# Kernel tuning notes

Hardware: AMD Instinct MI355X
Metric: run time of the kernel (lower is better)

## Reference

```python
import jax, jax.numpy as jnp
import numpy as np

N = 100000          # nodes of type 'note'
E = 800000          # edges per relation
D = 128             # in_feat == hidden_channels
NUM_LAYERS = 3
NUM_REL = 3         # onset, consecutive, during


def setup_inputs() -> dict:
    key = jax.random.key(0)
    ks = jax.random.split(key, 12)
    inp = {
        "x": jax.random.normal(ks[0], (N, D), dtype=jnp.float32),
        "edge_index_onset": jax.random.randint(ks[1], (2, E), 0, N, dtype=jnp.int64),
        "edge_index_consecutive": jax.random.randint(ks[2], (2, E), 0, N, dtype=jnp.int64),
        "edge_index_during": jax.random.randint(ks[3], (2, E), 0, N, dtype=jnp.int64),
        # hop masks: sorted node hops (seeds first), edge hops in [0, num_layers]
        "node_mask": jnp.sort(jax.random.randint(ks[4], (N,), 0, NUM_LAYERS + 1, dtype=jnp.int64)),
        "edge_mask_onset": jax.random.randint(ks[5], (E,), 0, NUM_LAYERS + 1, dtype=jnp.int64),
        "edge_mask_consecutive": jax.random.randint(ks[6], (E,), 0, NUM_LAYERS + 1, dtype=jnp.int64),
        "edge_mask_during": jax.random.randint(ks[7], (E,), 0, NUM_LAYERS + 1, dtype=jnp.int64),
        # SAGEConv weights per (layer, relation): lin_l (with bias) on aggregated
        # neighbor mean, lin_r (no bias) on root features.
        "W_l": jax.random.normal(ks[8], (NUM_LAYERS, NUM_REL, D, D), dtype=jnp.float32) / np.sqrt(D),
        "b_l": jnp.zeros((NUM_LAYERS, NUM_REL, D), dtype=jnp.float32),
        "W_r": jax.random.normal(ks[9], (NUM_LAYERS, NUM_REL, D, D), dtype=jnp.float32) / np.sqrt(D),
    }
    return inp


def _hetero_sage_forward(x, edge_indices, node_mask, edge_masks, W_l, b_l, W_r):
    h = x
    for i in range(NUM_LAYERS):
        layer = NUM_LAYERS - i  # trim_to_layer(layer=num_layers - i, ...)
        nvalid = node_mask <= layer                      # [N] kept nodes this layer
        out = jnp.zeros((N, D), dtype=h.dtype)
        for t in range(NUM_REL):
            src, dst = edge_indices[t][0], edge_indices[t][1]
            evalid = (edge_masks[t] <= layer).astype(h.dtype)  # [E] kept edges
            msg = h[src] * evalid[:, None]                     # gather + mask  [E, D]
            agg = jax.ops.segment_sum(msg, dst, num_segments=N)          # [N, D]
            cnt = jax.ops.segment_sum(evalid, dst, num_segments=N)       # [N]
            mean = agg / jnp.maximum(cnt, 1.0)[:, None]
            # SAGEConv: lin_l(mean) + lin_r(x_root); HeteroConv aggr='sum' over relations
            out = out + mean @ W_l[i, t].T + b_l[i, t] + h @ W_r[i, t].T
        h = jnp.where(nvalid[:, None], jax.nn.relu(out), 0.0)
    return h


def reference(x, edge_index_onset, edge_index_consecutive, edge_index_during,
              node_mask, edge_mask_onset, edge_mask_consecutive, edge_mask_during,
              W_l, b_l, W_r):
    edge_indices = (edge_index_onset, edge_index_consecutive, edge_index_during)
    edge_masks = (edge_mask_onset, edge_mask_consecutive, edge_mask_during)
    return _hetero_sage_forward(x, edge_indices, node_mask, edge_masks, W_l, b_l, W_r)
```

## Files before the change

kernel.cpp:

```cpp
#include <hip/hip_runtime.h>

#define N_NODES 100000
#define N_EDGES 800000
#define D 128
#define SCAN_N (4 * N_NODES)
#define SCAN_TOTAL (3 * SCAN_N)
#define SCAN_CHUNK 2048
#define SCAN_BLOCKS 586
#define SCAN_PAD (SCAN_BLOCKS * SCAN_CHUNK)

typedef _Float16 f16x8 __attribute__((ext_vector_type(8)));
typedef _Float16 f16x4 __attribute__((ext_vector_type(4)));
typedef float f32x4 __attribute__((ext_vector_type(4)));

#define MFMA_F16(a, b, c) __builtin_amdgcn_mfma_f32_16x16x32_f16((a), (b), (c), 0, 0, 0)

#define CONV_BLOCKS 12500
#define COUNT_BLOCKS 9375
#define PREPW_BLOCKS 768

__global__ __launch_bounds__(256) void prep_all(
    const float* __restrict__ x, _Float16* __restrict__ h,
    const int* __restrict__ ei0, const int* __restrict__ ei1, const int* __restrict__ ei2,
    const int* __restrict__ em0, const int* __restrict__ em1, const int* __restrict__ em2,
    int* __restrict__ cnt2, const float* __restrict__ W_l, const float* __restrict__ W_r,
    const float* __restrict__ b_l, _Float16* __restrict__ whi, float* __restrict__ bsum) {
    int b = blockIdx.x;
    int tid = threadIdx.x;
    if (b < CONV_BLOCKS) {
        int idx = b * 256 + tid;
        float4 v = reinterpret_cast<const float4*>(x)[idx];
        f16x4 o = {(_Float16)v.x, (_Float16)v.y, (_Float16)v.z, (_Float16)v.w};
        reinterpret_cast<f16x4*>(h)[idx] = o;
    } else if (b < CONV_BLOCKS + COUNT_BLOCKS) {
        int e = (b - CONV_BLOCKS) * 256 + tid;
        int r = e / N_EDGES;
        int el = e - r * N_EDGES;
        const int* ei = (r == 0) ? ei0 : (r == 1) ? ei1 : ei2;
        const int* em = (r == 0) ? em0 : (r == 1) ? em1 : em2;
        int dst = ei[N_EDGES + el];
        int m = em[el];
        atomicAdd(&cnt2[(size_t)r * SCAN_N + dst * 4 + m], 1);
    } else {
        int idx = (b - CONV_BLOCKS - COUNT_BLOCKS) * 256 + tid;
        if (idx < 3 * 4 * 16384) {
            int i = idx / (4 * 16384);
            int rem = idx % (4 * 16384);
            int slot = rem / 16384;
            int ok = rem % 16384;
            float v;
            if (slot < 3) {
                v = W_l[(size_t)(i * 3 + slot) * 16384 + ok];
            } else {
                const float* base = W_r + (size_t)i * 3 * 16384;
                v = base[ok] + base[16384 + ok] + base[2 * 16384 + ok];
            }
            whi[idx] = (_Float16)v;
        }
        if (idx < 3 * 128) {
            int i = idx / 128, o = idx % 128;
            const float* bb = b_l + (size_t)i * 3 * 128;
            bsum[idx] = bb[o] + bb[128 + o] + bb[256 + o];
        }
    }
}

__global__ __launch_bounds__(256) void scan_part(const int* __restrict__ cnt2,
                                                 int* __restrict__ bsums) {
    int tid = threadIdx.x;
    size_t base = (size_t)blockIdx.x * SCAN_CHUNK + tid * 8;
    int4 v0 = *reinterpret_cast<const int4*>(cnt2 + base);
    int4 v1 = *reinterpret_cast<const int4*>(cnt2 + base + 4);
    int s = v0.x + v0.y + v0.z + v0.w + v1.x + v1.y + v1.z + v1.w;
    __shared__ int red[256];
    red[tid] = s;
    __syncthreads();
    for (int off = 128; off > 0; off >>= 1) {
        if (tid < off) red[tid] += red[tid + off];
        __syncthreads();
    }
    if (tid == 0) bsums[blockIdx.x] = red[0];
}

__global__ __launch_bounds__(1024) void scan_tops(int* __restrict__ bsums) {
    __shared__ int s[1024];
    int tid = threadIdx.x;
    int v = (tid < SCAN_BLOCKS) ? bsums[tid] : 0;
    s[tid] = v;
    __syncthreads();
    for (int off = 1; off < 1024; off <<= 1) {
        int x = s[tid];
        int add = (tid >= off) ? s[tid - off] : 0;
        __syncthreads();
        s[tid] = x + add;
        __syncthreads();
    }
    if (tid < SCAN_BLOCKS) bsums[tid] = s[tid] - v;
}

__global__ __launch_bounds__(256) void scan_out(const int* __restrict__ cnt2,
                                                const int* __restrict__ bsums,
                                                int* __restrict__ bnd) {
    int tid = threadIdx.x;
    size_t base = (size_t)blockIdx.x * SCAN_CHUNK + tid * 8;
    int4 v0 = *reinterpret_cast<const int4*>(cnt2 + base);
    int4 v1 = *reinterpret_cast<const int4*>(cnt2 + base + 4);
    int l[8] = {v0.x, v0.y, v0.z, v0.w, v1.x, v1.y, v1.z, v1.w};
    int ts = l[0] + l[1] + l[2] + l[3] + l[4] + l[5] + l[6] + l[7];
    __shared__ int s[256];
    s[tid] = ts;
    __syncthreads();
    for (int off = 1; off < 256; off <<= 1) {
        int x = s[tid];
        int add = (tid >= off) ? s[tid - off] : 0;
        __syncthreads();
        s[tid] = x + add;
        __syncthreads();
    }
    int run = bsums[blockIdx.x] + s[tid] - ts;
    int o[8];
#pragma unroll
    for (int j = 0; j < 8; j++) {
        o[j] = run;
        run += l[j];
    }
    int4 o0 = {o[0], o[1], o[2], o[3]};
    int4 o1 = {o[4], o[5], o[6], o[7]};
    *reinterpret_cast<int4*>(bnd + base) = o0;
    *reinterpret_cast<int4*>(bnd + base + 4) = o1;
}

__global__ __launch_bounds__(256) void fill3(
    const int* __restrict__ ei0, const int* __restrict__ ei1, const int* __restrict__ ei2,
    const int* __restrict__ em0, const int* __restrict__ em1, const int* __restrict__ em2,
    const int* __restrict__ bnd, int* __restrict__ fill2, int* __restrict__ packed) {
    int e = blockIdx.x * 256 + threadIdx.x;
    int r = e / N_EDGES;
    int el = e - r * N_EDGES;
    const int* ei = (r == 0) ? ei0 : (r == 1) ? ei1 : ei2;
    const int* em = (r == 0) ? em0 : (r == 1) ? em1 : em2;
    int dst = ei[N_EDGES + el];
    int src = ei[el];
    int m = em[el];
    int gbk = r * SCAN_N + dst * 4 + m;
    int pos = bnd[gbk] + atomicAdd(&fill2[gbk], 1);
    packed[pos] = src * D;
}

__global__ __launch_bounds__(256, 8) void fused_layer(
    const _Float16* __restrict__ h_in, const int* __restrict__ bnd,
    const int* __restrict__ packed, const _Float16* __restrict__ Whi,
    const float* __restrict__ bias, const int* __restrict__ node_mask, int layer,
    _Float16* __restrict__ h_out, float* __restrict__ out_f32) {
    __shared__ __align__(16) _Float16 smean[3][32][136];
    int tid = threadIdx.x;
    int wid = tid >> 6;
    int lane = tid & 63;
    int row0 = blockIdx.x * 32;

    if (node_mask[row0] > layer) {
        if (out_f32) {
            f32x4 z = {0.f, 0.f, 0.f, 0.f};
            f32x4* o = reinterpret_cast<f32x4*>(out_f32 + (size_t)row0 * D);
#pragma unroll
            for (int k = 0; k < 4; k++) o[tid + k * 256] = z;
        } else {
            f16x8 z = (f16x8)(_Float16)0;
            f16x8* o = reinterpret_cast<f16x8*>(h_out + (size_t)row0 * D);
#pragma unroll
            for (int k = 0; k < 2; k++) o[tid + k * 256] = z;
        }
        return;
    }

    int g = lane >> 4;
    int l = lane & 15;

    const _Float16* hbase = h_in + l * 8;
#pragma unroll 1
    for (int it = 0; it < 6; it++) {
        int t = wid * 24 + it * 4 + g;
        int r = t >> 5;
        int n = t & 31;
        if (node_mask[row0 + n] > layer) continue;
        const int* B = bnd + (size_t)r * SCAN_N + (row0 + n) * 4;
        int beg = B[0];
        int end = B[layer + 1];
        int deg = end - beg;
        f16x8 acc = (f16x8)(_Float16)0;
#pragma unroll 1
        for (int e4 = beg & ~3; e4 < end; e4 += 4) {
            int4 s4 = *reinterpret_cast<const int4*>(packed + e4);
            if (e4 >= beg && e4 + 4 <= end) {
                f16x8 v0 = *reinterpret_cast<const f16x8*>(hbase + (size_t)(uint)s4.x);
                f16x8 v1 = *reinterpret_cast<const f16x8*>(hbase + (size_t)(uint)s4.y);
                f16x8 v2 = *reinterpret_cast<const f16x8*>(hbase + (size_t)(uint)s4.z);
                f16x8 v3 = *reinterpret_cast<const f16x8*>(hbase + (size_t)(uint)s4.w);
                acc += v0;
                acc += v1;
                acc += v2;
                acc += v3;
            } else {
                int ss[4] = {s4.x, s4.y, s4.z, s4.w};
#pragma unroll
                for (int j = 0; j < 4; j++) {
                    int e = e4 + j;
                    if (e >= beg && e < end)
                        acc += *reinterpret_cast<const f16x8*>(hbase + (size_t)(uint)ss[j]);
                }
            }
        }
        float inv = 1.f / fmaxf((float)deg, 1.f);
        f16x8 mv;
#pragma unroll
        for (int k = 0; k < 8; k++) mv[k] = (_Float16)((float)acc[k] * inv);
        *reinterpret_cast<f16x8*>(&smean[r][n][l * 8]) = mv;
    }
    __syncthreads();

    int colbase = wid * 32;
    int ln15 = lane & 15;
    int lg = lane >> 4;
    f32x4 acc[2][2] = {};

#pragma unroll
    for (int p = 0; p < 4; p++) {
        const _Float16* Whp = Whi + (size_t)p * 16384 + (size_t)colbase * D;
#pragma unroll
        for (int ks = 0; ks < 4; ks++) {
            int kof = ks * 32 + lg * 8;
            f16x8 a0f, a1f;
            if (p < 3) {
                a0f = *reinterpret_cast<const f16x8*>(&smean[p][ln15][kof]);
                a1f = *reinterpret_cast<const f16x8*>(&smean[p][16 + ln15][kof]);
            } else {
                a0f = *reinterpret_cast<const f16x8*>(h_in + (size_t)(row0 + ln15) * D + kof);
                a1f = *reinterpret_cast<const f16x8*>(h_in + (size_t)(row0 + 16 + ln15) * D + kof);
            }
            f16x8 bh0 = *reinterpret_cast<const f16x8*>(Whp + (size_t)ln15 * D + kof);
            f16x8 bh1 = *reinterpret_cast<const f16x8*>(Whp + (size_t)(16 + ln15) * D + kof);
            acc[0][0] = MFMA_F16(a0f, bh0, acc[0][0]);
            acc[0][1] = MFMA_F16(a0f, bh1, acc[0][1]);
            acc[1][0] = MFMA_F16(a1f, bh0, acc[1][0]);
            acc[1][1] = MFMA_F16(a1f, bh1, acc[1][1]);
        }
    }

#pragma unroll
    for (int r = 0; r < 2; r++)
#pragma unroll
        for (int j = 0; j < 4; j++) {
            int row = row0 + r * 16 + lg * 4 + j;
            bool valid = node_mask[row] <= layer;
#pragma unroll
            for (int cc = 0; cc < 2; cc++) {
                int col = colbase + cc * 16 + ln15;
                float v = acc[r][cc][j] + bias[col];
                v = valid ? fmaxf(v, 0.f) : 0.f;
                if (out_f32)
                    out_f32[(size_t)row * D + col] = v;
                else
                    h_out[(size_t)row * D + col] = (_Float16)v;
            }
        }
}

extern "C" void kernel_launch(void* const* d_in, const int* in_sizes, int n_in,
                              void* d_out, int out_size, void* d_ws, size_t ws_size,
                              hipStream_t stream) {
    const float* x = (const float*)d_in[0];
    const int* ei0 = (const int*)d_in[1];
    const int* ei1 = (const int*)d_in[2];
    const int* ei2 = (const int*)d_in[3];
    const int* node_mask = (const int*)d_in[4];
    const int* em0 = (const int*)d_in[5];
    const int* em1 = (const int*)d_in[6];
    const int* em2 = (const int*)d_in[7];
    const float* W_l = (const float*)d_in[8];
    const float* b_l = (const float*)d_in[9];
    const float* W_r = (const float*)d_in[10];

    _Float16* hA = (_Float16*)d_ws;
    _Float16* hB = hA + (size_t)N_NODES * D;
    _Float16* whi = hB + (size_t)N_NODES * D;
    float* bsum = (float*)(whi + 3 * 4 * 16384);
    int* cnt2 = (int*)(bsum + 3 * 128);
    int* fill2 = cnt2 + SCAN_PAD;
    int* bsums = fill2 + SCAN_TOTAL;
    int* bnd = bsums + 640;
    int* packed = bnd + SCAN_PAD;

    hipMemsetAsync(cnt2, 0, (size_t)(SCAN_PAD + SCAN_TOTAL) * sizeof(int), stream);

    prep_all<<<CONV_BLOCKS + COUNT_BLOCKS + PREPW_BLOCKS, 256, 0, stream>>>(
        x, hA, ei0, ei1, ei2, em0, em1, em2, cnt2, W_l, W_r, b_l, whi, bsum);
    scan_part<<<SCAN_BLOCKS, 256, 0, stream>>>(cnt2, bsums);
    scan_tops<<<1, 1024, 0, stream>>>(bsums);
    scan_out<<<SCAN_BLOCKS, 256, 0, stream>>>(cnt2, bsums, bnd);
    fill3<<<COUNT_BLOCKS, 256, 0, stream>>>(ei0, ei1, ei2, em0, em1, em2, bnd, fill2, packed);

    _Float16* hin = hA;
    _Float16* hout = hB;
    for (int i = 0; i < 3; i++) {
        int layer = 3 - i;
        float* of = (i == 2) ? (float*)d_out : nullptr;
        fused_layer<<<N_NODES / 32, 256, 0, stream>>>(
            hin, bnd, packed, whi + (size_t)i * 4 * 16384,
            bsum + (size_t)i * 128, node_mask, layer, hout, of);
        _Float16* tmp = hin; hin = hout; hout = tmp;
    }
}
```

Baseline: 631.9 us.

## Quantize node features to int8 per row for neighbor gather

```diff
diff --git a/kernel.cpp b/kernel.cpp
--- a/kernel.cpp
+++ b/kernel.cpp
@@ -11,6 +11,7 @@
 
 typedef _Float16 f16x8 __attribute__((ext_vector_type(8)));
 typedef _Float16 f16x4 __attribute__((ext_vector_type(4)));
+typedef _Float16 f16x2 __attribute__((ext_vector_type(2)));
 typedef float f32x4 __attribute__((ext_vector_type(4)));
 
 #define MFMA_F16(a, b, c) __builtin_amdgcn_mfma_f32_16x16x32_f16((a), (b), (c), 0, 0, 0)
@@ -65,6 +66,24 @@
     }
 }
 
+__global__ __launch_bounds__(256) void quant_rows(const _Float16* __restrict__ h,
+                                                  char* __restrict__ q,
+                                                  float* __restrict__ scales) {
+    int row = blockIdx.x * 4 + (threadIdx.x >> 6);
+    int lane = threadIdx.x & 63;
+    f16x2 v = *reinterpret_cast<const f16x2*>(h + (size_t)row * D + lane * 2);
+    float a0 = (float)v.x, a1 = (float)v.y;
+    float m = fmaxf(fabsf(a0), fabsf(a1));
+#pragma unroll
+    for (int off = 32; off; off >>= 1) m = fmaxf(m, __shfl_xor(m, off));
+    float k = (m > 0.f) ? 127.f / m : 0.f;
+    int q0 = (int)rintf(a0 * k);
+    int q1 = (int)rintf(a1 * k);
+    ushort pk = (ushort)((q0 & 0xFF) | ((q1 & 0xFF) << 8));
+    *reinterpret_cast<ushort*>(q + (size_t)row * D + lane * 2) = pk;
+    if (lane == 0) scales[row] = m * (1.f / 127.f);
+}
+
 __global__ __launch_bounds__(256) void scan_part(const int* __restrict__ cnt2,
                                                  int* __restrict__ bsums) {
     int tid = threadIdx.x;
@@ -147,8 +166,18 @@
     packed[pos] = src * D;
 }
 
-__global__ __launch_bounds__(256, 8) void fused_layer(
-    const _Float16* __restrict__ h_in, const int* __restrict__ bnd,
+__device__ __forceinline__ void acc8(float* a, uint2 b, float s) {
+#pragma unroll
+    for (int k = 0; k < 4; k++)
+        a[k] = fmaf(s, (float)((int)(b.x << (24 - 8 * k)) >> 24), a[k]);
+#pragma unroll
+    for (int k = 0; k < 4; k++)
+        a[4 + k] = fmaf(s, (float)((int)(b.y << (24 - 8 * k)) >> 24), a[4 + k]);
+}
+
+__global__ __launch_bounds__(256, 6) void fused_layer(
+    const _Float16* __restrict__ h_in, const char* __restrict__ q_in,
+    const float* __restrict__ scales, const int* __restrict__ bnd,
     const int* __restrict__ packed, const _Float16* __restrict__ Whi,
     const float* __restrict__ bias, const int* __restrict__ node_mask, int layer,
     _Float16* __restrict__ h_out, float* __restrict__ out_f32) {
@@ -176,7 +205,7 @@
     int g = lane >> 4;
     int l = lane & 15;
 
-    const _Float16* hbase = h_in + l * 8;
+    const char* qbase = q_in + l * 8;
 #pragma unroll 1
     for (int it = 0; it < 6; it++) {
         int t = wid * 24 + it * 4 + g;
@@ -187,33 +216,40 @@
         int beg = B[0];
         int end = B[layer + 1];
         int deg = end - beg;
-        f16x8 acc = (f16x8)(_Float16)0;
+        float a[8] = {};
 #pragma unroll 1
         for (int e4 = beg & ~3; e4 < end; e4 += 4) {
             int4 s4 = *reinterpret_cast<const int4*>(packed + e4);
             if (e4 >= beg && e4 + 4 <= end) {
-                f16x8 v0 = *reinterpret_cast<const f16x8*>(hbase + (size_t)(uint)s4.x);
-                f16x8 v1 = *reinterpret_cast<const f16x8*>(hbase + (size_t)(uint)s4.y);
-                f16x8 v2 = *reinterpret_cast<const f16x8*>(hbase + (size_t)(uint)s4.z);
-                f16x8 v3 = *reinterpret_cast<const f16x8*>(hbase + (size_t)(uint)s4.w);
-                acc += v0;
-                acc += v1;
-                acc += v2;
-                acc += v3;
+                uint2 b0 = *reinterpret_cast<const uint2*>(qbase + (size_t)(uint)s4.x);
+                uint2 b1 = *reinterpret_cast<const uint2*>(qbase + (size_t)(uint)s4.y);
+                uint2 b2 = *reinterpret_cast<const uint2*>(qbase + (size_t)(uint)s4.z);
+                uint2 b3 = *reinterpret_cast<const uint2*>(qbase + (size_t)(uint)s4.w);
+                float f0 = scales[(uint)s4.x >> 7];
+                float f1 = scales[(uint)s4.y >> 7];
+                float f2 = scales[(uint)s4.z >> 7];
+                float f3 = scales[(uint)s4.w >> 7];
+                acc8(a, b0, f0);
+                acc8(a, b1, f1);
+                acc8(a, b2, f2);
+                acc8(a, b3, f3);
             } else {
                 int ss[4] = {s4.x, s4.y, s4.z, s4.w};
 #pragma unroll
                 for (int j = 0; j < 4; j++) {
                     int e = e4 + j;
-                    if (e >= beg && e < end)
-                        acc += *reinterpret_cast<const f16x8*>(hbase + (size_t)(uint)ss[j]);
+                    if (e >= beg && e < end) {
+                        uint2 b = *reinterpret_cast<const uint2*>(qbase + (size_t)(uint)ss[j]);
+                        float f = scales[(uint)ss[j] >> 7];
+                        acc8(a, b, f);
+                    }
                 }
             }
         }
         float inv = 1.f / fmaxf((float)deg, 1.f);
         f16x8 mv;
 #pragma unroll
-        for (int k = 0; k < 8; k++) mv[k] = (_Float16)((float)acc[k] * inv);
+        for (int k = 0; k < 8; k++) mv[k] = (_Float16)(a[k] * inv);
         *reinterpret_cast<f16x8*>(&smean[r][n][l * 8]) = mv;
     }
     __syncthreads();
@@ -282,7 +318,11 @@
 
     _Float16* hA = (_Float16*)d_ws;
     _Float16* hB = hA + (size_t)N_NODES * D;
-    _Float16* whi = hB + (size_t)N_NODES * D;
+    char* qA = (char*)(hB + (size_t)N_NODES * D);
+    char* qB = qA + (size_t)N_NODES * D;
+    float* scA = (float*)(qB + (size_t)N_NODES * D);
+    float* scB = scA + N_NODES;
+    _Float16* whi = (_Float16*)(scB + N_NODES);
     float* bsum = (float*)(whi + 3 * 4 * 16384);
     int* cnt2 = (int*)(bsum + 3 * 128);
     int* fill2 = cnt2 + SCAN_PAD;
@@ -294,19 +334,20 @@
 
     prep_all<<<CONV_BLOCKS + COUNT_BLOCKS + PREPW_BLOCKS, 256, 0, stream>>>(
         x, hA, ei0, ei1, ei2, em0, em1, em2, cnt2, W_l, W_r, b_l, whi, bsum);
+    quant_rows<<<N_NODES / 4, 256, 0, stream>>>(hA, qA, scA);
     scan_part<<<SCAN_BLOCKS, 256, 0, stream>>>(cnt2, bsums);
     scan_tops<<<1, 1024, 0, stream>>>(bsums);
     scan_out<<<SCAN_BLOCKS, 256, 0, stream>>>(cnt2, bsums, bnd);
     fill3<<<COUNT_BLOCKS, 256, 0, stream>>>(ei0, ei1, ei2, em0, em1, em2, bnd, fill2, packed);
 
-    _Float16* hin = hA;
-    _Float16* hout = hB;
-    for (int i = 0; i < 3; i++) {
-        int layer = 3 - i;
-        float* of = (i == 2) ? (float*)d_out : nullptr;
-        fused_layer<<<N_NODES / 32, 256, 0, stream>>>(
-            hin, bnd, packed, whi + (size_t)i * 4 * 16384,
-            bsum + (size_t)i * 128, node_mask, layer, hout, of);
-        _Float16* tmp = hin; hin = hout; hout = tmp;
-    }
-}
+    fused_layer<<<N_NODES / 32, 256, 0, stream>>>(
+        hA, qA, scA, bnd, packed, whi, bsum, node_mask, 3, hB, nullptr);
+    quant_rows<<<N_NODES / 4, 256, 0, stream>>>(hB, qB, scB);
+    fused_layer<<<N_NODES / 32, 256, 0, stream>>>(
+        hB, qB, scB, bnd, packed, whi + (size_t)1 * 4 * 16384,
+        bsum + 128, node_mask, 2, hA, nullptr);
+    quant_rows<<<N_NODES / 4, 256, 0, stream>>>(hA, qA, scA);
+    fused_layer<<<N_NODES / 32, 256, 0, stream>>>(
+        hA, qA, scA, bnd, packed, whi + (size_t)2 * 4 * 16384,
+        bsum + 256, node_mask, 1, nullptr, (float*)d_out);
+}
```

Result: slower. 681.6 us (+7.9%).
